# Kernel optimization log

Hardware: AMD Instinct MI355X
Metric: run time of the kernel (lower is better)

## Reference

```python
import jax, jax.numpy as jnp
import numpy as np

ALPHA = 0.2          # leaky relu negative slope
SCALE_ATT = 1.0
NEG_MASK = -9e15


def setup_inputs() -> dict:
    key = jax.random.key(0)
    k1, k2, k3, k4 = jax.random.split(key, 4)
    B, N, Din, Dout = 32, 1024, 256, 256
    h = jax.random.normal(k1, (B, N, Din), dtype=jnp.float32)
    adj = jax.random.randint(k2, (B, N, N), 0, 2, dtype=jnp.int32)
    W = jax.random.normal(k3, (Dout, Din), dtype=jnp.float32) * (1.0 / np.sqrt(Din))
    b = jnp.zeros((Dout,), dtype=jnp.float32)
    a = jax.random.normal(k4, (2 * Dout,), dtype=jnp.float32) * 0.1
    return {"h": h, "adj": adj, "W": W, "b": b, "a": a}


def reference(h, adj, W, b, a):
    # z: [B, N, Dout]
    z = jnp.einsum('bnd,od->bno', h, W) + b
    Dout = z.shape[-1]
    a1, a2 = a[:Dout], a[Dout:]
    # a^T [z_i || z_j] = a1.z_i + a2.z_j  (same math as the N^2 concat)
    s1 = jnp.einsum('bnd,d->bn', z, a1)  # source score per node
    s2 = jnp.einsum('bnd,d->bn', z, a2)  # target score per node
    e = jax.nn.leaky_relu(s1[:, :, None] + s2[:, None, :], negative_slope=ALPHA)
    e = jnp.where(adj > 0, e, NEG_MASK) * SCALE_ATT
    attention = jax.nn.softmax(e, axis=-1)   # [B, N, N]
    # dropout p=0 / eval mode: no-op
    h_prime = jnp.einsum('bij,bjd->bid', attention, z)
    return jax.nn.elu(h_prime)
```

## Files before the change

### kernel.cpp

```cpp
#include <hip/hip_runtime.h>
#include <math.h>

#define LRELU_ALPHA 0.2f
#define NEG_MASK_V -9000000000000000.0f

typedef __attribute__((ext_vector_type(8))) short short8;
typedef __attribute__((ext_vector_type(4))) float floatx4;
typedef __attribute__((ext_vector_type(8))) unsigned short u16x8;
typedef __attribute__((ext_vector_type(4))) unsigned short u16x4;

__device__ __forceinline__ unsigned short f2bf(float x) {
  union { float f; unsigned u; } v; v.f = x;
  unsigned r = v.u + 0x7fff + ((v.u >> 16) & 1);
  return (unsigned short)(r >> 16);
}

__device__ __forceinline__ unsigned cvt_pk_bf16(float lo, float hi) {
  unsigned r;
  asm("v_cvt_pk_bf16_f32 %0, %1, %2" : "=v"(r) : "v"(lo), "v"(hi));
  return r;
}

__global__ __launch_bounds__(256) void prep_kernel(
    const float* __restrict__ W, const float* __restrict__ b,
    const float* __restrict__ a, unsigned short* __restrict__ Wb,
    float* __restrict__ u1, float* __restrict__ u2, float* __restrict__ cst)
{
  const int t = threadIdx.x;
  if (blockIdx.x == 0) {
    float a1s = 0.f, a2s = 0.f;
    #pragma unroll 4
    for (int o = 0; o < 256; ++o) {
      const float w = W[o * 256 + t];
      a1s = fmaf(w, a[o], a1s);
      a2s = fmaf(w, a[256 + o], a2s);
    }
    u1[t] = a1s; u2[t] = a2s;
    if (t < 64) {
      float p1 = 0.f, p2 = 0.f;
      #pragma unroll
      for (int q = 0; q < 4; ++q) {
        const float bv = b[t + q * 64];
        p1 = fmaf(bv, a[t + q * 64], p1);
        p2 = fmaf(bv, a[256 + t + q * 64], p2);
      }
      #pragma unroll
      for (int off = 32; off > 0; off >>= 1) {
        p1 += __shfl_xor(p1, off); p2 += __shfl_xor(p2, off);
      }
      if (t == 0) { cst[0] = p1; cst[1] = p2; }
    }
  } else {
    const int base = (blockIdx.x - 1) * 2048 + t * 8;
    const float4 v0 = *(const float4*)&W[base];
    const float4 v1 = *(const float4*)&W[base + 4];
    u16x8 o;
    o[0] = f2bf(v0.x); o[1] = f2bf(v0.y); o[2] = f2bf(v0.z); o[3] = f2bf(v0.w);
    o[4] = f2bf(v1.x); o[5] = f2bf(v1.y); o[6] = f2bf(v1.z); o[7] = f2bf(v1.w);
    *(u16x8*)&Wb[base] = o;
  }
}

__global__ __launch_bounds__(256) void sdot_kernel(
    const float* __restrict__ h, const float* __restrict__ u1,
    const float* __restrict__ u2, const float* __restrict__ cst,
    float* __restrict__ s1, float* __restrict__ s2)
{
  const int t = threadIdx.x, l = t & 63, w = t >> 6;
  const long row0 = (long)blockIdx.x * 64 + w * 16;
  const float4 u1v = *(const float4*)&u1[l * 4];
  const float4 u2v = *(const float4*)&u2[l * 4];
  const float c1 = cst[0], c2 = cst[1];
  #pragma unroll
  for (int r = 0; r < 16; ++r) {
    const float4 hv = *(const float4*)&h[(row0 + r) * 256 + l * 4];
    float d1 = hv.x * u1v.x + hv.y * u1v.y + hv.z * u1v.z + hv.w * u1v.w;
    float d2 = hv.x * u2v.x + hv.y * u2v.y + hv.z * u2v.z + hv.w * u2v.w;
    #pragma unroll
    for (int off = 32; off > 0; off >>= 1) {
      d1 += __shfl_xor(d1, off); d2 += __shfl_xor(d2, off);
    }
    if (l == 0) { s1[row0 + r] = d1 + c1; s2[row0 + r] = d2 + c2; }
  }
}

__global__ __launch_bounds__(256) void zmfma_kernel(
    const float* __restrict__ h, const unsigned short* __restrict__ Wb,
    const float* __restrict__ bias, unsigned short* __restrict__ zf)
{
  __shared__ __align__(16) unsigned char smem[46080];
  unsigned short (*h_tile)[72] = (unsigned short(*)[72])smem;
  unsigned short (*w_tile)[72] = (unsigned short(*)[72])(smem + 9216);
  unsigned short (*ztile)[68]  = (unsigned short(*)[68])smem;

  const int t = threadIdx.x, l = t & 63, w = t >> 6;
  const int bi = blockIdx.x;
  const long row0 = (long)bi * 64;

  floatx4 acc[4][4];
  #pragma unroll
  for (int mf = 0; mf < 4; ++mf)
    #pragma unroll
    for (int nf = 0; nf < 4; ++nf) acc[mf][nf] = (floatx4)0.f;

  for (int k0 = 0; k0 < 256; k0 += 64) {
    __syncthreads();
    #pragma unroll
    for (int p = 0; p < 4; ++p) {
      const int row = p * 16 + (t >> 4);
      const float4 hv = *(const float4*)&h[(row0 + row) * 256 + k0 + (t & 15) * 4];
      u16x4 hb;
      hb[0] = f2bf(hv.x); hb[1] = f2bf(hv.y); hb[2] = f2bf(hv.z); hb[3] = f2bf(hv.w);
      *(u16x4*)&h_tile[row][(t & 15) * 4] = hb;
    }
    #pragma unroll
    for (int p = 0; p < 8; ++p) {
      const int o = p * 32 + (t >> 3);
      const u16x8 wv = *(const u16x8*)&Wb[o * 256 + k0 + (t & 7) * 8];
      *(u16x8*)&w_tile[o][(t & 7) * 8] = wv;
    }
    __syncthreads();

    #pragma unroll
    for (int kk = 0; kk < 2; ++kk) {
      short8 af[4];
      #pragma unroll
      for (int mf = 0; mf < 4; ++mf)
        af[mf] = *(const short8*)&h_tile[mf * 16 + (l & 15)][kk * 32 + (l >> 4) * 8];
      #pragma unroll
      for (int nf = 0; nf < 4; ++nf) {
        const short8 bf = *(const short8*)&w_tile[w * 64 + nf * 16 + (l & 15)][kk * 32 + (l >> 4) * 8];
        #pragma unroll
        for (int mf = 0; mf < 4; ++mf)
          acc[mf][nf] = __builtin_amdgcn_mfma_f32_16x16x32_bf16(af[mf], bf, acc[mf][nf], 0, 0, 0);
      }
    }
  }

  __syncthreads();
  #pragma unroll
  for (int nf = 0; nf < 4; ++nf) {
    const int o = w * 64 + nf * 16 + (l & 15);
    const float bv = bias[o];
    #pragma unroll
    for (int mf = 0; mf < 4; ++mf) {
      uint2 zv;
      zv.x = cvt_pk_bf16(acc[mf][nf][0] + bv, acc[mf][nf][1] + bv);
      zv.y = cvt_pk_bf16(acc[mf][nf][2] + bv, acc[mf][nf][3] + bv);
      *(uint2*)&ztile[o][mf * 16 + (l >> 4) * 4] = zv;
    }
  }
  __syncthreads();
  #pragma unroll
  for (int seg = 0; seg < 8; ++seg)
    *(u16x8*)&zf[((size_t)bi * 8 + seg) * 2048 + t * 8] =
        *(const u16x8*)&ztile[t][seg * 8];
}

__global__ __launch_bounds__(512, 4) void attn_kernel(
    const unsigned short* __restrict__ zf, const float* __restrict__ s1g,
    const float* __restrict__ s2g, const int* __restrict__ adj,
    float* __restrict__ out)
{
  __shared__ unsigned short p_lds[2][64][72];
  __shared__ float s2s[1024];
  __shared__ float s1s[64];
  __shared__ float sum_lds[64];

  const int t = threadIdx.x;
  const int l = t & 63;
  const int w = t >> 6;

  const int wg = blockIdx.x;
  const int sw = (wg & 7) * 64 + (wg >> 3);
  const int b = sw >> 4;
  const int i0 = (sw & 15) * 64;

  const int i_loc = t >> 3;
  const int jb = (t & 7) * 8;

  const size_t adj_base = (size_t)b * 1024 * 1024 + (size_t)(i0 + i_loc) * 1024 + jb;
  const size_t zf_batch = (size_t)b * 16 * 16384;
  const size_t zf_lane  = (size_t)(l >> 4) * 2048 + (size_t)(w * 32 + (l & 15)) * 8;

  if (t < 64) s1s[t] = s1g[b * 1024 + i0 + t];
  s2s[t] = s2g[b * 1024 + t];
  s2s[512 + t] = s2g[b * 1024 + 512 + t];

  floatx4 acc[4][2];
  #pragma unroll
  for (int mf = 0; mf < 4; ++mf) {
    acc[mf][0] = (floatx4)0.f;
    acc[mf][1] = (floatx4)0.f;
  }
  float sm = 0.f;

  int4 ac[2][2];
  ac[0][0] = *(const int4*)&adj[adj_base];
  ac[0][1] = *(const int4*)&adj[adj_base + 4];
  ac[1][0] = *(const int4*)&adj[adj_base + 64];
  ac[1][1] = *(const int4*)&adj[adj_base + 68];

  short8 vz[2][4];
  {
    const unsigned short* zp = zf + zf_batch + zf_lane;
    vz[0][0] = *(const short8*)(zp);
    vz[0][1] = *(const short8*)(zp + 128);
    vz[0][2] = *(const short8*)(zp + 8192);
    vz[0][3] = *(const short8*)(zp + 8320);
  }
  __syncthreads();
  const float s1v = s1s[i_loc];

  for (int jt2 = 0; jt2 < 1024; jt2 += 128) {
    #pragma unroll
    for (int ph = 0; ph < 2; ++ph) {
      const int jt = jt2 + ph * 64;

      const float4 s2a = *(const float4*)&s2s[jt + jb];
      const float4 s2b = *(const float4*)&s2s[jt + jb + 4];
      const int4 a0 = ac[ph][0], a1 = ac[ph][1];
      float e[8] = {s2a.x, s2a.y, s2a.z, s2a.w, s2b.x, s2b.y, s2b.z, s2b.w};
      const int am[8] = {a0.x, a0.y, a0.z, a0.w, a1.x, a1.y, a1.z, a1.w};
      #pragma unroll
      for (int q = 0; q < 8; ++q) {
        float x = s1v + e[q];
        x = fmaxf(x, LRELU_ALPHA * x);
        e[q] = am[q] > 0 ? x : NEG_MASK_V;
      }

      if (jt + 128 < 1024) {
        ac[ph][0] = *(const int4*)&adj[adj_base + jt + 128];
        ac[ph][1] = *(const int4*)&adj[adj_base + jt + 132];
      }
      if (jt + 64 < 1024) {
        const unsigned short* zp =
            zf + zf_batch + (size_t)((jt >> 6) + 1) * 16384 + zf_lane;
        vz[ph ^ 1][0] = *(const short8*)(zp);
        vz[ph ^ 1][1] = *(const short8*)(zp + 128);
        vz[ph ^ 1][2] = *(const short8*)(zp + 8192);
        vz[ph ^ 1][3] = *(const short8*)(zp + 8320);
      }

      float p[8];
      #pragma unroll
      for (int q = 0; q < 8; ++q) { p[q] = __expf(e[q]); sm += p[q]; }
      uint4 pk;
      pk.x = cvt_pk_bf16(p[0], p[1]);
      pk.y = cvt_pk_bf16(p[2], p[3]);
      pk.z = cvt_pk_bf16(p[4], p[5]);
      pk.w = cvt_pk_bf16(p[6], p[7]);
      *(uint4*)&p_lds[ph][i_loc][jb] = pk;

      asm volatile("s_waitcnt lgkmcnt(0)" ::: "memory");
      __builtin_amdgcn_s_barrier();
      __builtin_amdgcn_sched_barrier(0);

      __builtin_amdgcn_s_setprio(1);
      #pragma unroll
      for (int kk = 0; kk < 2; ++kk) {
        #pragma unroll
        for (int mf = 0; mf < 4; ++mf) {
          const short8 af =
              *(const short8*)&p_lds[ph][mf * 16 + (l & 15)][kk * 32 + (l >> 4) * 8];
          acc[mf][0] = __builtin_amdgcn_mfma_f32_16x16x32_bf16(
              af, vz[ph][kk * 2 + 0], acc[mf][0], 0, 0, 0);
          acc[mf][1] = __builtin_amdgcn_mfma_f32_16x16x32_bf16(
              af, vz[ph][kk * 2 + 1], acc[mf][1], 0, 0, 0);
        }
      }
      __builtin_amdgcn_s_setprio(0);
    }
  }

  sm += __shfl_xor(sm, 1);
  sm += __shfl_xor(sm, 2);
  sm += __shfl_xor(sm, 4);
  if ((t & 7) == 0) sum_lds[i_loc] = sm;
  __syncthreads();

  const size_t obase = ((size_t)b * 1024 + i0) * 256 + w * 32;
  #pragma unroll
  for (int mf = 0; mf < 4; ++mf) {
    const int rbase = mf * 16 + ((l >> 4) << 2);
    #pragma unroll
    for (int rg = 0; rg < 4; ++rg) {
      const float inv = 1.0f / sum_lds[rbase + rg];
      #pragma unroll
      for (int nf = 0; nf < 2; ++nf) {
        float v = acc[mf][nf][rg] * inv;
        v = v > 0.f ? v : expm1f(v);
        out[obase + (size_t)(rbase + rg) * 256 + nf * 16 + (l & 15)] = v;
      }
    }
  }
}

extern "C" void kernel_launch(void* const* d_in, const int* in_sizes, int n_in,
                              void* d_out, int out_size, void* d_ws, size_t ws_size,
                              hipStream_t stream) {
  const float* h    = (const float*)d_in[0];
  const int*   adj  = (const int*)d_in[1];
  const float* W    = (const float*)d_in[2];
  const float* bias = (const float*)d_in[3];
  const float* a    = (const float*)d_in[4];
  float* out = (float*)d_out;

  unsigned short* zf = (unsigned short*)d_ws;
  float* s1  = (float*)((char*)d_ws + 16777216);
  float* s2  = (float*)((char*)d_ws + 16908288);
  float* u1  = (float*)((char*)d_ws + 17039360);
  float* u2  = (float*)((char*)d_ws + 17040384);
  float* cst = (float*)((char*)d_ws + 17041408);
  unsigned short* Wb = (unsigned short*)((char*)d_ws + 17825792);

  prep_kernel<<<dim3(33), dim3(256), 0, stream>>>(W, bias, a, Wb, u1, u2, cst);
  sdot_kernel<<<dim3(512), dim3(256), 0, stream>>>(h, u1, u2, cst, s1, s2);
  zmfma_kernel<<<dim3(512), dim3(256), 0, stream>>>(h, Wb, bias, zf);
  attn_kernel<<<dim3(512), dim3(512), 0, stream>>>(zf, s1, s2, adj, out);
}
```

Measured before the change: 76.31 us.

## Prepack adjacency into LDS bitmask up front and single-buffer P tile

Each block now reads its whole 64x1024 adjacency slab at the start with nontemporal loads and compresses it into a per-row bitmask in LDS. This replaces the per-iteration register-prefetched int4 loads inside the loop. P is single-buffered with two __syncthreads per step instead of the double buffer with one barrier and setprio. Output stores become nontemporal. The goal is to stream adjacency in one burst and cut register pressure, at the cost of no overlap between the adjacency read and compute and an extra barrier per tile.

```diff
diff --git a/kernel.cpp b/kernel.cpp
--- a/kernel.cpp
+++ b/kernel.cpp
@@ -8,6 +8,7 @@
 typedef __attribute__((ext_vector_type(4))) float floatx4;
 typedef __attribute__((ext_vector_type(8))) unsigned short u16x8;
 typedef __attribute__((ext_vector_type(4))) unsigned short u16x4;
+typedef __attribute__((ext_vector_type(4))) int i32x4;
 
 __device__ __forceinline__ unsigned short f2bf(float x) {
   union { float f; unsigned u; } v; v.f = x;
@@ -162,7 +163,8 @@
     const float* __restrict__ s2g, const int* __restrict__ adj,
     float* __restrict__ out)
 {
-  __shared__ unsigned short p_lds[2][64][72];
+  __shared__ unsigned short p_lds[64][72];
+  __shared__ unsigned bits_lds[64][33];
   __shared__ float s2s[1024];
   __shared__ float s1s[64];
   __shared__ float sum_lds[64];
@@ -179,7 +181,6 @@
   const int i_loc = t >> 3;
   const int jb = (t & 7) * 8;
 
-  const size_t adj_base = (size_t)b * 1024 * 1024 + (size_t)(i0 + i_loc) * 1024 + jb;
   const size_t zf_batch = (size_t)b * 16 * 16384;
   const size_t zf_lane  = (size_t)(l >> 4) * 2048 + (size_t)(w * 32 + (l & 15)) * 8;
 
@@ -187,6 +188,25 @@
   s2s[t] = s2g[b * 1024 + t];
   s2s[512 + t] = s2g[b * 1024 + 512 + t];
 
+  {
+    const size_t adj_b = (size_t)b * 1024 * 1024;
+    #pragma unroll
+    for (int p = 0; p < 4; ++p) {
+      const int r = p * 16 + (t >> 5);
+      const int* rowp = adj + adj_b + (size_t)(i0 + r) * 1024 + (t & 31) * 32;
+      unsigned bits = 0;
+      #pragma unroll
+      for (int q = 0; q < 8; ++q) {
+        const i32x4 v = __builtin_nontemporal_load((const i32x4*)(rowp + q * 4));
+        bits |= (unsigned)(v.x > 0) << (q * 4);
+        bits |= (unsigned)(v.y > 0) << (q * 4 + 1);
+        bits |= (unsigned)(v.z > 0) << (q * 4 + 2);
+        bits |= (unsigned)(v.w > 0) << (q * 4 + 3);
+      }
+      bits_lds[r][t & 31] = bits;
+    }
+  }
+
   floatx4 acc[4][2];
   #pragma unroll
   for (int mf = 0; mf < 4; ++mf) {
@@ -194,12 +214,6 @@
     acc[mf][1] = (floatx4)0.f;
   }
   float sm = 0.f;
-
-  int4 ac[2][2];
-  ac[0][0] = *(const int4*)&adj[adj_base];
-  ac[0][1] = *(const int4*)&adj[adj_base + 4];
-  ac[1][0] = *(const int4*)&adj[adj_base + 64];
-  ac[1][1] = *(const int4*)&adj[adj_base + 68];
 
   short8 vz[2][4];
   {
@@ -217,22 +231,19 @@
     for (int ph = 0; ph < 2; ++ph) {
       const int jt = jt2 + ph * 64;
 
+      const unsigned wbits = bits_lds[i_loc][2 * (jt >> 6) + ((t & 7) >> 2)];
+      const unsigned mbyte = (wbits >> (((t & 7) & 3) * 8)) & 0xffu;
+
       const float4 s2a = *(const float4*)&s2s[jt + jb];
       const float4 s2b = *(const float4*)&s2s[jt + jb + 4];
-      const int4 a0 = ac[ph][0], a1 = ac[ph][1];
       float e[8] = {s2a.x, s2a.y, s2a.z, s2a.w, s2b.x, s2b.y, s2b.z, s2b.w};
-      const int am[8] = {a0.x, a0.y, a0.z, a0.w, a1.x, a1.y, a1.z, a1.w};
       #pragma unroll
       for (int q = 0; q < 8; ++q) {
         float x = s1v + e[q];
         x = fmaxf(x, LRELU_ALPHA * x);
-        e[q] = am[q] > 0 ? x : NEG_MASK_V;
-      }
-
-      if (jt + 128 < 1024) {
-        ac[ph][0] = *(const int4*)&adj[adj_base + jt + 128];
-        ac[ph][1] = *(const int4*)&adj[adj_base + jt + 132];
-      }
+        e[q] = (mbyte & (1u << q)) ? x : NEG_MASK_V;
+      }
+
       if (jt + 64 < 1024) {
         const unsigned short* zp =
             zf + zf_batch + (size_t)((jt >> 6) + 1) * 16384 + zf_lane;
@@ -250,26 +261,23 @@
       pk.y = cvt_pk_bf16(p[2], p[3]);
       pk.z = cvt_pk_bf16(p[4], p[5]);
       pk.w = cvt_pk_bf16(p[6], p[7]);
-      *(uint4*)&p_lds[ph][i_loc][jb] = pk;
-
-      asm volatile("s_waitcnt lgkmcnt(0)" ::: "memory");
-      __builtin_amdgcn_s_barrier();
-      __builtin_amdgcn_sched_barrier(0);
-
-      __builtin_amdgcn_s_setprio(1);
+
+      __syncthreads();
+      *(uint4*)&p_lds[i_loc][jb] = pk;
+      __syncthreads();
+
       #pragma unroll
       for (int kk = 0; kk < 2; ++kk) {
         #pragma unroll
         for (int mf = 0; mf < 4; ++mf) {
           const short8 af =
-              *(const short8*)&p_lds[ph][mf * 16 + (l & 15)][kk * 32 + (l >> 4) * 8];
+              *(const short8*)&p_lds[mf * 16 + (l & 15)][kk * 32 + (l >> 4) * 8];
           acc[mf][0] = __builtin_amdgcn_mfma_f32_16x16x32_bf16(
               af, vz[ph][kk * 2 + 0], acc[mf][0], 0, 0, 0);
           acc[mf][1] = __builtin_amdgcn_mfma_f32_16x16x32_bf16(
               af, vz[ph][kk * 2 + 1], acc[mf][1], 0, 0, 0);
         }
       }
-      __builtin_amdgcn_s_setprio(0);
     }
   }
 
@@ -290,7 +298,8 @@
       for (int nf = 0; nf < 2; ++nf) {
         float v = acc[mf][nf][rg] * inv;
         v = v > 0.f ? v : expm1f(v);
-        out[obase + (size_t)(rbase + rg) * 256 + nf * 16 + (l & 15)] = v;
+        __builtin_nontemporal_store(
+            v, &out[obase + (size_t)(rbase + rg) * 256 + nf * 16 + (l & 15)]);
       }
     }
   }
```

Result: slower. 156.2 us (+104.7%).
